# Performance work log

Measured on AMD Instinct MI355X. Metric: run time of the kernel, lower is better.

Reference implementation:

```python
import jax, jax.numpy as jnp
import numpy as np

N, F, O = 8192, 1024, 1024
NUM_NEIGH = 10


def setup_inputs() -> dict:
    key = jax.random.key(0)
    k1, k2, k3, k4, k5 = jax.random.split(key, 5)
    X = jax.random.normal(k1, (N, F), dtype=jnp.float32)
    A = jax.random.uniform(k2, (N, N), dtype=jnp.float32)
    stdv = 1.0 / np.sqrt(O)
    W = jax.random.uniform(k3, (2 * F, O), dtype=jnp.float32, minval=-stdv, maxval=stdv)
    b = jax.random.uniform(k4, (O,), dtype=jnp.float32, minval=-stdv, maxval=stdv)
    # Uniform neighbor sampling (original uses np.random.choice over range(N) per node)
    sampled_idx = jax.random.randint(k5, (N, NUM_NEIGH), 0, N, dtype=jnp.int32)
    return {"X": X, "A": A, "W": W, "b": b, "sampled_idx": sampled_idx}


def reference(X, A, W, b, sampled_idx):
    # aggregate: mean of uniformly sampled neighbor features per node.
    # (The matrix_power of the normalized A in the original is dead code; A's
    #  values never influence the output.)
    gathered = X[sampled_idx]                 # [N, num_neigh, F]
    aggregated = jnp.mean(gathered, axis=1)   # [N, F]
    combined = jnp.concatenate([X, aggregated], axis=1)  # [N, 2F]
    return combined @ W + b                   # [N, O]
```

## Files before the change

### kernel.cpp

```cpp
#include <hip/hip_runtime.h>
#include <stdint.h>

#define NN 8192
#define FD 1024
#define OD 1024
#define KD 2048
#define NB 10

typedef short bf16x8 __attribute__((ext_vector_type(8)));
typedef float f32x4  __attribute__((ext_vector_type(4)));

static __device__ __forceinline__ float bf2f(ushort u) {
  union { uint32_t i; float f; } v; v.i = ((uint32_t)u) << 16; return v.f;
}
static __device__ __forceinline__ ushort f2bf(float f) {
  union { float f; uint32_t i; } v; v.f = f;
  uint32_t x = v.i;
  return (ushort)((x + 0x7FFFu + ((x >> 16) & 1u)) >> 16);
}
static __device__ __forceinline__ bf16x8 cvt8(const float* p) {
  const float4 a = *reinterpret_cast<const float4*>(p);
  const float4 b = *reinterpret_cast<const float4*>(p + 4);
  bf16x8 v;
  v[0] = (short)f2bf(a.x); v[1] = (short)f2bf(a.y);
  v[2] = (short)f2bf(a.z); v[3] = (short)f2bf(a.w);
  v[4] = (short)f2bf(b.x); v[5] = (short)f2bf(b.y);
  v[6] = (short)f2bf(b.z); v[7] = (short)f2bf(b.w);
  return v;
}

static __device__ __forceinline__ void async16(const ushort* g, ushort* l) {
  __builtin_amdgcn_global_load_lds(
      (const __attribute__((address_space(1))) uint32_t*)(const void*)g,
      (__attribute__((address_space(3))) uint32_t*)(void*)l, 16, 0, 0);
}

__global__ __launch_bounds__(256) void xconv(const float* __restrict__ X,
                                             ushort* __restrict__ Ab) {
  const int q   = blockIdx.x * 256 + threadIdx.x;
  const int row = q >> 7;
  const int col = (q & 127) * 8;
  const bf16x8 v = cvt8(X + (size_t)row * FD + col);
  *reinterpret_cast<bf16x8*>(Ab + (size_t)row * KD + col) = v;
}

__global__ __launch_bounds__(256) void aggk(const int* __restrict__ idx,
                                            ushort* __restrict__ Ab) {
  const int row  = blockIdx.x * 2 + (threadIdx.x >> 7);
  const int lane = threadIdx.x & 127;
  const int col  = lane * 8;
  const int* ip = idx + (size_t)row * NB;
  int nb[NB];
#pragma unroll
  for (int j = 0; j < NB; ++j) nb[j] = ip[j];
  float acc[8] = {0.f, 0.f, 0.f, 0.f, 0.f, 0.f, 0.f, 0.f};
#pragma unroll
  for (int j = 0; j < NB; ++j) {
    const uint4 v = *reinterpret_cast<const uint4*>(Ab + (size_t)nb[j] * KD + col);
    const ushort* u = reinterpret_cast<const ushort*>(&v);
#pragma unroll
    for (int e = 0; e < 8; ++e) acc[e] += bf2f(u[e]);
  }
  bf16x8 o;
#pragma unroll
  for (int e = 0; e < 8; ++e) o[e] = (short)f2bf(acc[e] * 0.1f);
  *reinterpret_cast<bf16x8*>(Ab + (size_t)row * KD + FD + col) = o;
}

__global__ __launch_bounds__(1024) void wconv(const float* __restrict__ W,
                                              ushort* __restrict__ Wtb) {
  __shared__ float tile[64][65];
  const int k0 = blockIdx.x * 64;
  const int n0 = blockIdx.y * 64;
  const int tx = threadIdx.x;
  const int ty = threadIdx.y;
#pragma unroll
  for (int r = 0; r < 4; ++r) {
    const int kl = ty + r * 16;
    tile[kl][tx] = W[(size_t)(k0 + kl) * OD + n0 + tx];
  }
  __syncthreads();
#pragma unroll
  for (int r = 0; r < 4; ++r) {
    const int nl = ty + r * 16;
    Wtb[(size_t)(n0 + nl) * KD + k0 + tx] = f2bf(tile[tx][nl]);
  }
}

__global__ __launch_bounds__(256, 2) void gemm_fast3(const ushort* __restrict__ Ab,
                                                     const ushort* __restrict__ Wtb,
                                                     const float* __restrict__ Bias,
                                                     float* __restrict__ Out) {
  __shared__ ushort lA[128 * 64];
  __shared__ ushort lB[128 * 64];
  const int t  = threadIdx.x;
  const int id  = blockIdx.x;
  const int xcd = id & 7;
  const int j   = id >> 3;
  const int m0  = (xcd * 8 + (j >> 3)) * 128;
  const int n0  = (j & 7) * 128;

  const int wave = t >> 6;
  const int lane = t & 63;
  const int wm   = (wave & 1) * 64;
  const int wn   = (wave >> 1) * 64;
  const int l15  = lane & 15;
  const int quad = lane >> 4;

  f32x4 acc[4][4];
#pragma unroll
  for (int i = 0; i < 4; ++i)
#pragma unroll
    for (int jj = 0; jj < 4; ++jj) acc[i][jj] = (f32x4){0.f, 0.f, 0.f, 0.f};

  const ushort* gA[4];
  const ushort* gB[4];
#pragma unroll
  for (int i = 0; i < 4; ++i) {
    const int q   = i * 256 + t;
    const int row = q >> 3;
    const int ch  = q & 7;
    const int c   = (ch - row) & 7;
    gA[i] = Ab  + (size_t)(m0 + row) * KD + c * 8;
    gB[i] = Wtb + (size_t)(n0 + row) * KD + c * 8;
  }

  for (int k0 = 0; k0 < KD; k0 += 64) {
#pragma unroll
    for (int i = 0; i < 4; ++i) {
      async16(gA[i] + k0, lA + (i * 256 + t) * 8);
      async16(gB[i] + k0, lB + (i * 256 + t) * 8);
    }
    __syncthreads();

#pragma unroll
    for (int s = 0; s < 2; ++s) {
      const int c = s * 4 + quad;
      bf16x8 afr[4], bfr[4];
#pragma unroll
      for (int mi = 0; mi < 4; ++mi) {
        const int r = wm + mi * 16 + l15;
        afr[mi] = *reinterpret_cast<const bf16x8*>(lA + r * 64 + ((c + r) & 7) * 8);
      }
#pragma unroll
      for (int ni = 0; ni < 4; ++ni) {
        const int r = wn + ni * 16 + l15;
        bfr[ni] = *reinterpret_cast<const bf16x8*>(lB + r * 64 + ((c + r) & 7) * 8);
      }
#pragma unroll
      for (int mi = 0; mi < 4; ++mi)
#pragma unroll
        for (int ni = 0; ni < 4; ++ni)
          acc[mi][ni] = __builtin_amdgcn_mfma_f32_16x16x32_bf16(afr[mi], bfr[ni], acc[mi][ni], 0, 0, 0);
    }
    __syncthreads();
  }

#pragma unroll
  for (int ni = 0; ni < 4; ++ni) {
    const int gn = n0 + wn + ni * 16 + l15;
    const float bv = Bias[gn];
#pragma unroll
    for (int mi = 0; mi < 4; ++mi) {
      const int gm = m0 + wm + mi * 16 + quad * 4;
#pragma unroll
      for (int r = 0; r < 4; ++r)
        Out[(size_t)(gm + r) * OD + gn] = acc[mi][ni][r] + bv;
    }
  }
}

__global__ __launch_bounds__(256) void gemm_fused(const float* __restrict__ X,
                                                  const float* __restrict__ W,
                                                  const float* __restrict__ Bias,
                                                  const int* __restrict__ idx,
                                                  float* __restrict__ Out) {
  __shared__ ushort lA[128 * 32];
  __shared__ ushort lB[32 * 128];
  const int t    = threadIdx.x;
  const int m0   = blockIdx.y * 128;
  const int n0   = blockIdx.x * 128;
  const int wave = t >> 6;
  const int lane = t & 63;
  const int wm   = (wave & 1) * 64;
  const int wn   = (wave >> 1) * 64;
  const int l15  = lane & 15;
  const int quad = lane >> 4;

  f32x4 acc[4][4];
#pragma unroll
  for (int i = 0; i < 4; ++i)
#pragma unroll
    for (int j = 0; j < 4; ++j) acc[i][j] = (f32x4){0.f, 0.f, 0.f, 0.f};

  for (int kt = 0; kt < KD / 32; ++kt) {
    const int k0 = kt * 32;
    if (k0 < FD) {
#pragma unroll
      for (int r = 0; r < 2; ++r) {
        const int q = r * 256 + t;
        const int row = q >> 2, ch = q & 3;
        *reinterpret_cast<bf16x8*>(lA + q * 8) =
            cvt8(X + (size_t)(m0 + row) * FD + k0 + ch * 8);
      }
    } else {
      const int kc = k0 - FD;
#pragma unroll
      for (int r = 0; r < 2; ++r) {
        const int q = r * 256 + t;
        const int row = q >> 2, ch = q & 3;
        float a8[8] = {0.f, 0.f, 0.f, 0.f, 0.f, 0.f, 0.f, 0.f};
        const int* ip = idx + (size_t)(m0 + row) * NB;
#pragma unroll
        for (int j = 0; j < NB; ++j) {
          const float* p = X + (size_t)ip[j] * FD + kc + ch * 8;
          const float4 a = *(const float4*)p;
          const float4 b = *(const float4*)(p + 4);
          a8[0] += a.x; a8[1] += a.y; a8[2] += a.z; a8[3] += a.w;
          a8[4] += b.x; a8[5] += b.y; a8[6] += b.z; a8[7] += b.w;
        }
        bf16x8 v;
#pragma unroll
        for (int e = 0; e < 8; ++e) v[e] = (short)f2bf(a8[e] * 0.1f);
        *reinterpret_cast<bf16x8*>(lA + q * 8) = v;
      }
    }
#pragma unroll
    for (int r = 0; r < 2; ++r) {
      const int q = r * 256 + t;
      const int kr = q >> 4, ch = q & 15;
      *reinterpret_cast<bf16x8*>(lB + q * 8) =
          cvt8(W + (size_t)(k0 + kr) * OD + n0 + ch * 8);
    }
    __syncthreads();

    bf16x8 afr[4], bfr[4];
#pragma unroll
    for (int mi = 0; mi < 4; ++mi)
      afr[mi] = *reinterpret_cast<const bf16x8*>(lA + (wm + mi * 16 + l15) * 32 + quad * 8);
#pragma unroll
    for (int ni = 0; ni < 4; ++ni) {
      const int col = wn + ni * 16 + l15;
#pragma unroll
      for (int j = 0; j < 8; ++j)
        bfr[ni][j] = (short)lB[(quad * 8 + j) * 128 + col];
    }
#pragma unroll
    for (int mi = 0; mi < 4; ++mi)
#pragma unroll
      for (int ni = 0; ni < 4; ++ni)
        acc[mi][ni] = __builtin_amdgcn_mfma_f32_16x16x32_bf16(afr[mi], bfr[ni], acc[mi][ni], 0, 0, 0);
    __syncthreads();
  }
#pragma unroll
  for (int ni = 0; ni < 4; ++ni) {
    const int gn = n0 + wn + ni * 16 + l15;
    const float bv = Bias[gn];
#pragma unroll
    for (int mi = 0; mi < 4; ++mi) {
      const int gm = m0 + wm + mi * 16 + quad * 4;
#pragma unroll
      for (int r = 0; r < 4; ++r)
        Out[(size_t)(gm + r) * OD + gn] = acc[mi][ni][r] + bv;
    }
  }
}

extern "C" void kernel_launch(void* const* d_in, const int* in_sizes, int n_in,
                              void* d_out, int out_size, void* d_ws, size_t ws_size,
                              hipStream_t stream) {
  const float* X   = (const float*)d_in[0];
  const float* W   = (const float*)d_in[2];
  const float* b   = (const float*)d_in[3];
  const int*   idx = (const int*)d_in[4];
  float* out = (float*)d_out;

  const size_t need = ((size_t)NN * KD + (size_t)OD * KD) * sizeof(ushort);
  if (ws_size >= need) {
    ushort* Ab  = (ushort*)d_ws;
    ushort* Wtb = Ab + (size_t)NN * KD;

    xconv<<<NN * FD / (256 * 8), 256, 0, stream>>>(X, Ab);
    wconv<<<dim3(KD / 64, OD / 64), dim3(64, 16), 0, stream>>>(W, Wtb);
    aggk<<<NN / 2, 256, 0, stream>>>(idx, Ab);
    gemm_fast3<<<512, 256, 0, stream>>>(Ab, Wtb, b, out);
  } else {
    gemm_fused<<<dim3(OD / 128, NN / 128), 256, 0, stream>>>(X, W, b, idx, out);
  }
}
```

Before: 390.5 us.

## Drop workspace by staging bf16 operands inside output buffer with grid barrier

Removes the separate X conversion kernel and the workspace. The aggregated bf16 features and transposed bf16 W are now stored inside the output buffer itself. The GEMM converts X from fp32 to bf16 on the fly for the first K half and reads the staged aggregate for the second half. Before writing results it runs a spin-wait grid barrier, because staged data would otherwise be overwritten, and two output elements that hold the counters are written last. This saves the xconv pass and its traffic but depends on all 512 blocks being co-resident and adds synchronous fp32 loads in the first GEMM phase.

New measurement: 450.9 us. +15.4%, slower.

```diff
diff --git a/kernel.cpp b/kernel.cpp
--- a/kernel.cpp
+++ b/kernel.cpp
@@ -6,6 +6,7 @@
 #define OD 1024
 #define KD 2048
 #define NB 10
+#define NBLK 512
 
 typedef short bf16x8 __attribute__((ext_vector_type(8)));
 typedef float f32x4  __attribute__((ext_vector_type(4)));
@@ -35,41 +36,21 @@
       (__attribute__((address_space(3))) uint32_t*)(void*)l, 16, 0, 0);
 }
 
-__global__ __launch_bounds__(256) void xconv(const float* __restrict__ X,
-                                             ushort* __restrict__ Ab) {
-  const int q   = blockIdx.x * 256 + threadIdx.x;
-  const int row = q >> 7;
-  const int col = (q & 127) * 8;
-  const bf16x8 v = cvt8(X + (size_t)row * FD + col);
-  *reinterpret_cast<bf16x8*>(Ab + (size_t)row * KD + col) = v;
-}
-
-__global__ __launch_bounds__(256) void aggk(const int* __restrict__ idx,
-                                            ushort* __restrict__ Ab) {
-  const int row  = blockIdx.x * 2 + (threadIdx.x >> 7);
-  const int lane = threadIdx.x & 127;
-  const int col  = lane * 8;
-  const int* ip = idx + (size_t)row * NB;
-  int nb[NB];
-#pragma unroll
-  for (int j = 0; j < NB; ++j) nb[j] = ip[j];
-  float acc[8] = {0.f, 0.f, 0.f, 0.f, 0.f, 0.f, 0.f, 0.f};
-#pragma unroll
-  for (int j = 0; j < NB; ++j) {
-    const uint4 v = *reinterpret_cast<const uint4*>(Ab + (size_t)nb[j] * KD + col);
-    const ushort* u = reinterpret_cast<const ushort*>(&v);
-#pragma unroll
-    for (int e = 0; e < 8; ++e) acc[e] += bf2f(u[e]);
-  }
-  bf16x8 o;
-#pragma unroll
-  for (int e = 0; e < 8; ++e) o[e] = (short)f2bf(acc[e] * 0.1f);
-  *reinterpret_cast<bf16x8*>(Ab + (size_t)row * KD + FD + col) = o;
-}
-
-__global__ __launch_bounds__(1024) void wconv(const float* __restrict__ W,
-                                              ushort* __restrict__ Wtb) {
+static __device__ __forceinline__ int* ctr1_of(float* Out) {
+  return (int*)(Out + (size_t)5120 * OD);
+}
+static __device__ __forceinline__ int* ctr2_of(float* Out) {
+  return (int*)(Out + (size_t)5121 * OD);
+}
+
+__global__ __launch_bounds__(1024) void wprep(const float* __restrict__ W,
+                                              float* __restrict__ Out) {
   __shared__ float tile[64][65];
+  ushort* Wtb = (ushort*)Out + (size_t)NN * FD;
+  if (blockIdx.x == 0 && blockIdx.y == 0 && threadIdx.x == 0 && threadIdx.y == 0) {
+    __hip_atomic_store(ctr1_of(Out), 0, __ATOMIC_RELAXED, __HIP_MEMORY_SCOPE_AGENT);
+    __hip_atomic_store(ctr2_of(Out), 0, __ATOMIC_RELAXED, __HIP_MEMORY_SCOPE_AGENT);
+  }
   const int k0 = blockIdx.x * 64;
   const int n0 = blockIdx.y * 64;
   const int tx = threadIdx.x;
@@ -87,12 +68,41 @@
   }
 }
 
-__global__ __launch_bounds__(256, 2) void gemm_fast3(const ushort* __restrict__ Ab,
-                                                     const ushort* __restrict__ Wtb,
-                                                     const float* __restrict__ Bias,
-                                                     float* __restrict__ Out) {
+__global__ __launch_bounds__(256) void aggf(const float* __restrict__ X,
+                                            const int* __restrict__ idx,
+                                            float* __restrict__ Out) {
+  ushort* Agg = (ushort*)Out;
+  const int row = blockIdx.x * 2 + (threadIdx.x >> 7);
+  const int col = (threadIdx.x & 127) * 8;
+  const int* ip = idx + (size_t)row * NB;
+  int nb[NB];
+#pragma unroll
+  for (int j = 0; j < NB; ++j) nb[j] = ip[j];
+  float acc[8] = {0.f, 0.f, 0.f, 0.f, 0.f, 0.f, 0.f, 0.f};
+#pragma unroll
+  for (int j = 0; j < NB; ++j) {
+    const float* p = X + (size_t)nb[j] * FD + col;
+    const float4 a = *reinterpret_cast<const float4*>(p);
+    const float4 b = *reinterpret_cast<const float4*>(p + 4);
+    acc[0] += a.x; acc[1] += a.y; acc[2] += a.z; acc[3] += a.w;
+    acc[4] += b.x; acc[5] += b.y; acc[6] += b.z; acc[7] += b.w;
+  }
+  bf16x8 o;
+#pragma unroll
+  for (int e = 0; e < 8; ++e) o[e] = (short)f2bf(acc[e] * 0.1f);
+  *reinterpret_cast<bf16x8*>(Agg + (size_t)row * FD + col) = o;
+}
+
+__global__ __launch_bounds__(256, 2) void gemm_nws(const float* __restrict__ X,
+                                                   const float* __restrict__ Bias,
+                                                   float* __restrict__ Out) {
   __shared__ ushort lA[128 * 64];
   __shared__ ushort lB[128 * 64];
+  const ushort* Agg = (const ushort*)Out;
+  const ushort* Wtb = (const ushort*)Out + (size_t)NN * FD;
+  int* ctr1 = ctr1_of(Out);
+  int* ctr2 = ctr2_of(Out);
+
   const int t  = threadIdx.x;
   const int id  = blockIdx.x;
   const int xcd = id & 7;
@@ -113,6 +123,7 @@
 #pragma unroll
     for (int jj = 0; jj < 4; ++jj) acc[i][jj] = (f32x4){0.f, 0.f, 0.f, 0.f};
 
+  int rowq[4], cq[4];
   const ushort* gA[4];
   const ushort* gB[4];
 #pragma unroll
@@ -121,18 +132,21 @@
     const int row = q >> 3;
     const int ch  = q & 7;
     const int c   = (ch - row) & 7;
-    gA[i] = Ab  + (size_t)(m0 + row) * KD + c * 8;
+    rowq[i] = row; cq[i] = c;
+    gA[i] = Agg + (size_t)(m0 + row) * FD + c * 8;
     gB[i] = Wtb + (size_t)(n0 + row) * KD + c * 8;
   }
 
-  for (int k0 = 0; k0 < KD; k0 += 64) {
+  for (int k0 = 0; k0 < FD; k0 += 64) {
+#pragma unroll
+    for (int i = 0; i < 4; ++i)
+      async16(gB[i] + k0, lB + (i * 256 + t) * 8);
 #pragma unroll
     for (int i = 0; i < 4; ++i) {
-      async16(gA[i] + k0, lA + (i * 256 + t) * 8);
-      async16(gB[i] + k0, lB + (i * 256 + t) * 8);
-    }
-    __syncthreads();
-
+      const bf16x8 v = cvt8(X + (size_t)(m0 + rowq[i]) * FD + k0 + cq[i] * 8);
+      *reinterpret_cast<bf16x8*>(lA + (i * 256 + t) * 8) = v;
+    }
+    __syncthreads();
 #pragma unroll
     for (int s = 0; s < 2; ++s) {
       const int c = s * 4 + quad;
@@ -156,6 +170,47 @@
     __syncthreads();
   }
 
+  for (int k0 = 0; k0 < FD; k0 += 64) {
+#pragma unroll
+    for (int i = 0; i < 4; ++i) {
+      async16(gA[i] + k0, lA + (i * 256 + t) * 8);
+      async16(gB[i] + FD + k0, lB + (i * 256 + t) * 8);
+    }
+    __syncthreads();
+#pragma unroll
+    for (int s = 0; s < 2; ++s) {
+      const int c = s * 4 + quad;
+      bf16x8 afr[4], bfr[4];
+#pragma unroll
+      for (int mi = 0; mi < 4; ++mi) {
+        const int r = wm + mi * 16 + l15;
+        afr[mi] = *reinterpret_cast<const bf16x8*>(lA + r * 64 + ((c + r) & 7) * 8);
+      }
+#pragma unroll
+      for (int ni = 0; ni < 4; ++ni) {
+        const int r = wn + ni * 16 + l15;
+        bfr[ni] = *reinterpret_cast<const bf16x8*>(lB + r * 64 + ((c + r) & 7) * 8);
+      }
+#pragma unroll
+      for (int mi = 0; mi < 4; ++mi)
+#pragma unroll
+        for (int ni = 0; ni < 4; ++ni)
+          acc[mi][ni] = __builtin_amdgcn_mfma_f32_16x16x32_bf16(afr[mi], bfr[ni], acc[mi][ni], 0, 0, 0);
+    }
+    __syncthreads();
+  }
+
+  if (t == 0) {
+    __hip_atomic_fetch_add(ctr1, 1, __ATOMIC_ACQ_REL, __HIP_MEMORY_SCOPE_AGENT);
+    for (int it = 0; it < (1 << 21); ++it) {
+      if (__hip_atomic_load(ctr1, __ATOMIC_ACQUIRE, __HIP_MEMORY_SCOPE_AGENT) >= NBLK) break;
+      __builtin_amdgcn_s_sleep(8);
+    }
+    __hip_atomic_fetch_add(ctr2, 1, __ATOMIC_ACQ_REL, __HIP_MEMORY_SCOPE_AGENT);
+  }
+  __syncthreads();
+
+  const bool def5 = (id == 5) && (t == 0);
 #pragma unroll
   for (int ni = 0; ni < 4; ++ni) {
     const int gn = n0 + wn + ni * 16 + l15;
@@ -164,105 +219,20 @@
     for (int mi = 0; mi < 4; ++mi) {
       const int gm = m0 + wm + mi * 16 + quad * 4;
 #pragma unroll
-      for (int r = 0; r < 4; ++r)
+      for (int r = 0; r < 4; ++r) {
+        if (def5 && mi == 0 && ni == 0 && r < 2) continue;
         Out[(size_t)(gm + r) * OD + gn] = acc[mi][ni][r] + bv;
-    }
-  }
-}
-
-__global__ __launch_bounds__(256) void gemm_fused(const float* __restrict__ X,
-                                                  const float* __restrict__ W,
-                                                  const float* __restrict__ Bias,
-                                                  const int* __restrict__ idx,
-                                                  float* __restrict__ Out) {
-  __shared__ ushort lA[128 * 32];
-  __shared__ ushort lB[32 * 128];
-  const int t    = threadIdx.x;
-  const int m0   = blockIdx.y * 128;
-  const int n0   = blockIdx.x * 128;
-  const int wave = t >> 6;
-  const int lane = t & 63;
-  const int wm   = (wave & 1) * 64;
-  const int wn   = (wave >> 1) * 64;
-  const int l15  = lane & 15;
-  const int quad = lane >> 4;
-
-  f32x4 acc[4][4];
-#pragma unroll
-  for (int i = 0; i < 4; ++i)
-#pragma unroll
-    for (int j = 0; j < 4; ++j) acc[i][j] = (f32x4){0.f, 0.f, 0.f, 0.f};
-
-  for (int kt = 0; kt < KD / 32; ++kt) {
-    const int k0 = kt * 32;
-    if (k0 < FD) {
-#pragma unroll
-      for (int r = 0; r < 2; ++r) {
-        const int q = r * 256 + t;
-        const int row = q >> 2, ch = q & 3;
-        *reinterpret_cast<bf16x8*>(lA + q * 8) =
-            cvt8(X + (size_t)(m0 + row) * FD + k0 + ch * 8);
-      }
-    } else {
-      const int kc = k0 - FD;
-#pragma unroll
-      for (int r = 0; r < 2; ++r) {
-        const int q = r * 256 + t;
-        const int row = q >> 2, ch = q & 3;
-        float a8[8] = {0.f, 0.f, 0.f, 0.f, 0.f, 0.f, 0.f, 0.f};
-        const int* ip = idx + (size_t)(m0 + row) * NB;
-#pragma unroll
-        for (int j = 0; j < NB; ++j) {
-          const float* p = X + (size_t)ip[j] * FD + kc + ch * 8;
-          const float4 a = *(const float4*)p;
-          const float4 b = *(const float4*)(p + 4);
-          a8[0] += a.x; a8[1] += a.y; a8[2] += a.z; a8[3] += a.w;
-          a8[4] += b.x; a8[5] += b.y; a8[6] += b.z; a8[7] += b.w;
-        }
-        bf16x8 v;
-#pragma unroll
-        for (int e = 0; e < 8; ++e) v[e] = (short)f2bf(a8[e] * 0.1f);
-        *reinterpret_cast<bf16x8*>(lA + q * 8) = v;
-      }
-    }
-#pragma unroll
-    for (int r = 0; r < 2; ++r) {
-      const int q = r * 256 + t;
-      const int kr = q >> 4, ch = q & 15;
-      *reinterpret_cast<bf16x8*>(lB + q * 8) =
-          cvt8(W + (size_t)(k0 + kr) * OD + n0 + ch * 8);
-    }
-    __syncthreads();
-
-    bf16x8 afr[4], bfr[4];
-#pragma unroll
-    for (int mi = 0; mi < 4; ++mi)
-      afr[mi] = *reinterpret_cast<const bf16x8*>(lA + (wm + mi * 16 + l15) * 32 + quad * 8);
-#pragma unroll
-    for (int ni = 0; ni < 4; ++ni) {
-      const int col = wn + ni * 16 + l15;
-#pragma unroll
-      for (int j = 0; j < 8; ++j)
-        bfr[ni][j] = (short)lB[(quad * 8 + j) * 128 + col];
-    }
-#pragma unroll
-    for (int mi = 0; mi < 4; ++mi)
-#pragma unroll
-      for (int ni = 0; ni < 4; ++ni)
-        acc[mi][ni] = __builtin_amdgcn_mfma_f32_16x16x32_bf16(afr[mi], bfr[ni], acc[mi][ni], 0, 0, 0);
-    __syncthreads();
-  }
-#pragma unroll
-  for (int ni = 0; ni < 4; ++ni) {
-    const int gn = n0 + wn + ni * 16 + l15;
-    const float bv = Bias[gn];
-#pragma unroll
-    for (int mi = 0; mi < 4; ++mi) {
-      const int gm = m0 + wm + mi * 16 + quad * 4;
-#pragma unroll
-      for (int r = 0; r < 4; ++r)
-        Out[(size_t)(gm + r) * OD + gn] = acc[mi][ni][r] + bv;
-    }
+      }
+    }
+  }
+  if (def5) {
+    const float bv0 = Bias[0];
+    for (int it = 0; it < (1 << 21); ++it) {
+      if (__hip_atomic_load(ctr2, __ATOMIC_ACQUIRE, __HIP_MEMORY_SCOPE_AGENT) >= NBLK) break;
+      __builtin_amdgcn_s_sleep(8);
+    }
+    Out[(size_t)5120 * OD] = acc[0][0][0] + bv0;
+    Out[(size_t)5121 * OD] = acc[0][0][1] + bv0;
   }
 }
 
@@ -274,17 +244,9 @@
   const float* b   = (const float*)d_in[3];
   const int*   idx = (const int*)d_in[4];
   float* out = (float*)d_out;
-
-  const size_t need = ((size_t)NN * KD + (size_t)OD * KD) * sizeof(ushort);
-  if (ws_size >= need) {
-    ushort* Ab  = (ushort*)d_ws;
-    ushort* Wtb = Ab + (size_t)NN * KD;
-
-    xconv<<<NN * FD / (256 * 8), 256, 0, stream>>>(X, Ab);
-    wconv<<<dim3(KD / 64, OD / 64), dim3(64, 16), 0, stream>>>(W, Wtb);
-    aggk<<<NN / 2, 256, 0, stream>>>(idx, Ab);
-    gemm_fast3<<<512, 256, 0, stream>>>(Ab, Wtb, b, out);
-  } else {
-    gemm_fused<<<dim3(OD / 128, NN / 128), 256, 0, stream>>>(X, W, b, idx, out);
-  }
-}
+  (void)d_ws; (void)ws_size;
+
+  wprep<<<dim3(KD / 64, OD / 64), dim3(64, 16), 0, stream>>>(W, out);
+  aggf<<<NN / 2, 256, 0, stream>>>(X, idx, out);
+  gemm_nws<<<NBLK, 256, 0, stream>>>(X, b, out);
+}
```

## Use 256x128 GEMM tiles with triple-buffered async LDS pipeline

Applied to the files above, without the earlier changes.

The bf16 MFMA GEMM now uses 512-thread blocks computing 256x128 output tiles. Global-to-LDS loads are triple-buffered and issued three tiles ahead, with vmcnt waits replacing the full sync after each load. MFMA sections also raise wave priority. This is meant to hide global load latency and raise operand reuse, at the cost of 144KB LDS per block (lower occupancy) and fewer blocks (256) across the CUs.

Result: no change. 396.9 us (+1.6%).

```diff
diff --git a/kernel.cpp b/kernel.cpp
--- a/kernel.cpp
+++ b/kernel.cpp
@@ -87,23 +87,23 @@
   }
 }
 
-__global__ __launch_bounds__(256, 2) void gemm_fast3(const ushort* __restrict__ Ab,
-                                                     const ushort* __restrict__ Wtb,
-                                                     const float* __restrict__ Bias,
-                                                     float* __restrict__ Out) {
-  __shared__ ushort lA[128 * 64];
-  __shared__ ushort lB[128 * 64];
+__global__ __launch_bounds__(512, 2) void gemm_256x128(const ushort* __restrict__ Ab,
+                                                       const ushort* __restrict__ Wtb,
+                                                       const float* __restrict__ Bias,
+                                                       float* __restrict__ Out) {
+  __shared__ ushort lA[3 * 256 * 64];
+  __shared__ ushort lB[3 * 128 * 64];
   const int t  = threadIdx.x;
   const int id  = blockIdx.x;
   const int xcd = id & 7;
   const int j   = id >> 3;
-  const int m0  = (xcd * 8 + (j >> 3)) * 128;
+  const int m0  = (xcd * 4 + (j >> 3)) * 256;
   const int n0  = (j & 7) * 128;
 
   const int wave = t >> 6;
   const int lane = t & 63;
-  const int wm   = (wave & 1) * 64;
-  const int wn   = (wave >> 1) * 64;
+  const int wm   = (wave >> 1) * 64;
+  const int wn   = (wave & 1) * 64;
   const int l15  = lane & 15;
   const int quad = lane >> 4;
 
@@ -114,25 +114,35 @@
     for (int jj = 0; jj < 4; ++jj) acc[i][jj] = (f32x4){0.f, 0.f, 0.f, 0.f};
 
   const ushort* gA[4];
-  const ushort* gB[4];
+  const ushort* gB[2];
 #pragma unroll
   for (int i = 0; i < 4; ++i) {
-    const int q   = i * 256 + t;
+    const int q   = i * 512 + t;
     const int row = q >> 3;
-    const int ch  = q & 7;
-    const int c   = (ch - row) & 7;
-    gA[i] = Ab  + (size_t)(m0 + row) * KD + c * 8;
+    const int c   = ((q & 7) - row) & 7;
+    gA[i] = Ab + (size_t)(m0 + row) * KD + c * 8;
+  }
+#pragma unroll
+  for (int i = 0; i < 2; ++i) {
+    const int q   = i * 512 + t;
+    const int row = q >> 3;
+    const int c   = ((q & 7) - row) & 7;
     gB[i] = Wtb + (size_t)(n0 + row) * KD + c * 8;
   }
 
-  for (int k0 = 0; k0 < KD; k0 += 64) {
-#pragma unroll
-    for (int i = 0; i < 4; ++i) {
-      async16(gA[i] + k0, lA + (i * 256 + t) * 8);
-      async16(gB[i] + k0, lB + (i * 256 + t) * 8);
-    }
-    __syncthreads();
-
+  auto STAGE = [&](int tile, int buf) {
+    const int k0 = tile * 64;
+    ushort* la = lA + buf * (256 * 64);
+    ushort* lb = lB + buf * (128 * 64);
+#pragma unroll
+    for (int i = 0; i < 4; ++i) async16(gA[i] + k0, la + (i * 512 + t) * 8);
+#pragma unroll
+    for (int i = 0; i < 2; ++i) async16(gB[i] + k0, lb + (i * 512 + t) * 8);
+  };
+
+  auto COMPUTE = [&](int buf) {
+    const ushort* la = lA + buf * (256 * 64);
+    const ushort* lb = lB + buf * (128 * 64);
 #pragma unroll
     for (int s = 0; s < 2; ++s) {
       const int c = s * 4 + quad;
@@ -140,21 +150,41 @@
 #pragma unroll
       for (int mi = 0; mi < 4; ++mi) {
         const int r = wm + mi * 16 + l15;
-        afr[mi] = *reinterpret_cast<const bf16x8*>(lA + r * 64 + ((c + r) & 7) * 8);
+        afr[mi] = *reinterpret_cast<const bf16x8*>(la + r * 64 + ((c + r) & 7) * 8);
       }
 #pragma unroll
       for (int ni = 0; ni < 4; ++ni) {
         const int r = wn + ni * 16 + l15;
-        bfr[ni] = *reinterpret_cast<const bf16x8*>(lB + r * 64 + ((c + r) & 7) * 8);
+        bfr[ni] = *reinterpret_cast<const bf16x8*>(lb + r * 64 + ((c + r) & 7) * 8);
       }
+      __builtin_amdgcn_s_setprio(1);
 #pragma unroll
       for (int mi = 0; mi < 4; ++mi)
 #pragma unroll
         for (int ni = 0; ni < 4; ++ni)
           acc[mi][ni] = __builtin_amdgcn_mfma_f32_16x16x32_bf16(afr[mi], bfr[ni], acc[mi][ni], 0, 0, 0);
-    }
-    __syncthreads();
-  }
+      __builtin_amdgcn_s_setprio(0);
+    }
+  };
+
+  STAGE(0, 0); STAGE(1, 1); STAGE(2, 2);
+
+  int buf = 0;
+  for (int tile = 0; tile <= 28; ++tile) {
+    asm volatile("s_waitcnt vmcnt(12)\ns_barrier" ::: "memory");
+    COMPUTE(buf);
+    asm volatile("s_barrier" ::: "memory");
+    STAGE(tile + 3, buf);
+    buf = (buf == 2) ? 0 : buf + 1;
+  }
+  asm volatile("s_waitcnt vmcnt(12)\ns_barrier" ::: "memory");
+  COMPUTE(buf);
+  buf = (buf == 2) ? 0 : buf + 1;
+  asm volatile("s_waitcnt vmcnt(6)\ns_barrier" ::: "memory");
+  COMPUTE(buf);
+  buf = (buf == 2) ? 0 : buf + 1;
+  asm volatile("s_waitcnt vmcnt(0)\ns_barrier" ::: "memory");
+  COMPUTE(buf);
 
 #pragma unroll
   for (int ni = 0; ni < 4; ++ni) {
@@ -283,7 +313,7 @@
     xconv<<<NN * FD / (256 * 8), 256, 0, stream>>>(X, Ab);
     wconv<<<dim3(KD / 64, OD / 64), dim3(64, 16), 0, stream>>>(W, Wtb);
     aggk<<<NN / 2, 256, 0, stream>>>(idx, Ab);
-    gemm_fast3<<<512, 256, 0, stream>>>(Ab, Wtb, b, out);
+    gemm_256x128<<<256, 512, 0, stream>>>(Ab, Wtb, b, out);
   } else {
     gemm_fused<<<dim3(OD / 128, NN / 128), 256, 0, stream>>>(X, W, b, idx, out);
   }
```
